# Optimization experiments

Hardware: AMD Instinct MI355X
Metric: run time of the kernel (lower is better)

## Reference

```python
import jax, jax.numpy as jnp
import numpy as np

# Model dims (match init_kwargs)
D_MODEL = 2048
H = 16        # query heads
HKV = 4       # kv heads (GQA)
DS = 32       # semantic head dim (compressed)
DG = 32       # geometric head dim (compressed, RoPE'd)
DV = 64       # value head dim
B, T = 2, 4096
MB = 64       # mem_block
LW = 1024     # local_window
ROPE_BASE = 10000.0
NEG_INF = -1e9


def _rope(x, pos, base):
    # x: [B, h, T, d] with d even; standard rotate-half RoPE
    d = x.shape[-1]
    inv_freq = 1.0 / (base ** (jnp.arange(0, d, 2, dtype=jnp.float32) / d))
    ang = pos.astype(jnp.float32)[:, None] * inv_freq          # [T, d/2]
    cos, sin = jnp.cos(ang), jnp.sin(ang)                      # [T, d/2]
    x1, x2 = jnp.split(x, 2, axis=-1)
    return jnp.concatenate([x1 * cos - x2 * sin,
                            x2 * cos + x1 * sin], axis=-1)


def setup_inputs() -> dict:
    key = jax.random.key(0)
    ks = jax.random.split(key, 8)
    w = lambda k, sh: jax.random.normal(k, sh, jnp.float32) * 0.02
    return {
        "x": jax.random.normal(ks[0], (B, T, D_MODEL), jnp.float32),
        "Wq_sem": w(ks[1], (D_MODEL, H * DS)),
        "Wk_sem": w(ks[2], (D_MODEL, HKV * DS)),
        "Wq_geo": w(ks[3], (D_MODEL, H * DG)),
        "Wk_geo": w(ks[4], (D_MODEL, HKV * DG)),
        "Wv": w(ks[5], (D_MODEL, HKV * DV)),
        "Wo": w(ks[6], (H * DV, D_MODEL)),
        "logit_scale": jnp.zeros((H,), jnp.float32),
    }


def reference(x, Wq_sem, Wk_sem, Wq_geo, Wk_geo, Wv, Wo, logit_scale):
    Bq, Tq = x.shape[0], x.shape[1]
    split = lambda y, h, d: y.reshape(Bq, Tq, h, d).transpose(0, 2, 1, 3)
    # Decoupled projections
    q_sem = split(x @ Wq_sem, H, DS)      # [B,H,T,DS]
    k_sem = split(x @ Wk_sem, HKV, DS)    # [B,HKV,T,DS]
    q_geo = split(x @ Wq_geo, H, DG)
    k_geo = split(x @ Wk_geo, HKV, DG)
    v = split(x @ Wv, HKV, DV)            # [B,HKV,T,DV]
    pos = jnp.arange(Tq)
    # RoPE only on the geometric path
    q_geo = _rope(q_geo, pos, ROPE_BASE)
    k_geo = _rope(k_geo, pos, ROPE_BASE)
    # Memory-block summarization: mean-pool remote KV into one token per block
    remote = Tq - LW
    nblk = remote // MB
    pool = lambda a: jnp.concatenate(
        [a[:, :, :remote].reshape(Bq, HKV, nblk, MB, a.shape[-1]).mean(axis=3),
         a[:, :, remote:]], axis=2)
    k_sem2, k_geo2, v2 = pool(k_sem), pool(k_geo), pool(v)  # [B,HKV,K,*], K=nblk+LW
    k_pos = jnp.concatenate([jnp.arange(nblk) * MB + (MB - 1),
                             jnp.arange(remote, Tq)])        # [K]
    # GQA head-group broadcast
    rep = lambda a: jnp.repeat(a, H // HKV, axis=1)
    k_sem2, k_geo2, v2 = rep(k_sem2), rep(k_geo2), rep(v2)   # [B,H,K,*]
    # Decoupled scores: semantic + geometric, each with its own scale
    scores = (jnp.einsum('bhqd,bhkd->bhqk', q_sem, k_sem2) * (1.0 / jnp.sqrt(float(DS)))
              + jnp.einsum('bhqd,bhkd->bhqk', q_geo, k_geo2) * (1.0 / jnp.sqrt(float(DG))))
    # Learned per-head temperature
    scores = scores * jnp.exp(logit_scale)[None, :, None, None]
    # Causal mask over summarized key positions
    mask = k_pos[None, :] <= pos[:, None]                    # [T,K]
    scores = jnp.where(mask[None, None], scores, NEG_INF)
    probs = jax.nn.softmax(scores, axis=-1)
    out = jnp.einsum('bhqk,bhkd->bhqd', probs, v2)           # [B,H,T,DV]
    out = out.transpose(0, 2, 1, 3).reshape(Bq, Tq, H * DV)
    return out @ Wo                                          # [B,T,D_MODEL]
```

## Files before the change

kernel.cpp:

```cpp
#include <hip/hip_runtime.h>
#include <math.h>

#define B_  2
#define T_  4096
#define DM  2048
#define H_  16
#define HKV 4
#define DV_ 64
#define MB_ 64
#define LW_ 1024
#define REMOTE 3072
#define NBLK 48
#define KTOT 1072
#define NTILES 17

typedef __bf16 bf16x8 __attribute__((ext_vector_type(8)));
typedef float  f32x4  __attribute__((ext_vector_type(4)));

__device__ __forceinline__ float bf2f(unsigned short u) {
    unsigned int x = ((unsigned int)u) << 16;
    return __builtin_bit_cast(float, x);
}
__device__ __forceinline__ unsigned short f2bf(float f) {
    unsigned int x = __builtin_bit_cast(unsigned int, f);
    x = x + 0x7fffu + ((x >> 16) & 1u);
    return (unsigned short)(x >> 16);
}

__device__ __forceinline__ void gload16(const unsigned short* gsrc,
                                        unsigned short* ldst) {
    __builtin_amdgcn_global_load_lds(
        (const __attribute__((address_space(1))) void*)gsrc,
        (__attribute__((address_space(3))) void*)ldst,
        16, 0, 0);
}

__global__ void cvt_f32_to_bf16(const float* __restrict__ src,
                                unsigned short* __restrict__ dst, int n) {
    int i = (blockIdx.x * blockDim.x + threadIdx.x) * 4;
    if (i >= n) return;
    float4 v = *(const float4*)(src + i);
    ushort4 o;
    o.x = f2bf(v.x); o.y = f2bf(v.y); o.z = f2bf(v.z); o.w = f2bf(v.w);
    *(ushort4*)(dst + i) = o;
}

__global__ void transpose_cvt(const float* __restrict__ src,
                              unsigned short* __restrict__ dst, int R, int C) {
    __shared__ float tile[32][33];
    int ct = blockIdx.x, rt = blockIdx.y;
    int tx = threadIdx.x, ty = threadIdx.y;
    #pragma unroll
    for (int i = ty; i < 32; i += 8)
        tile[i][tx] = src[(size_t)(rt * 32 + i) * C + ct * 32 + tx];
    __syncthreads();
    #pragma unroll
    for (int i = ty; i < 32; i += 8)
        dst[(size_t)(ct * 32 + i) * R + rt * 32 + tx] = f2bf(tile[tx][i]);
}

template<int MODE>
__global__ __launch_bounds__(256, 3) void gemmP(
    const unsigned short* __restrict__ A,
    const unsigned short* __restrict__ BT,
    float* __restrict__ outF,
    unsigned short* __restrict__ qcat,
    unsigned short* __restrict__ kcatf,
    unsigned short* __restrict__ vf,
    int M, int N, int K, int nbx)
{
    extern __shared__ __align__(16) unsigned short lds[];

    const int tid = threadIdx.x;
    const int lane = tid & 63, w = tid >> 6;
    const int wr = w >> 1, wc = w & 1;
    const int l15 = lane & 15, lg = lane >> 4;

    const int cpx = gridDim.x >> 3;
    const int swz = (blockIdx.x & 7) * cpx + (blockIdx.x >> 3);
    const int bx = swz % nbx, by = swz / nbx;
    const int row0 = by * 128, col0 = bx * 128;

    const int scol = ((lane & 3) ^ ((lane >> 3) & 3)) * 8;
    const int srA = w * 16 + (lane >> 2);
    const unsigned short* Ag = A  + (size_t)row0 * K;
    const unsigned short* Bg = BT + (size_t)col0 * K;

    const int rdsw = (lg ^ ((l15 >> 1) & 3)) * 8;
    const int aoff = (wr * 64 + l15) * 32 + rdsw;
    const int boff = (wc * 64 + l15) * 32 + rdsw;

    const int NT = K >> 5;
    f32x4 acc[4][4] = {};

    auto stage = [&](int s, int kk) {
        unsigned short* sa = lds + s * 8192;
        unsigned short* sb = sa + 4096;
        #pragma unroll
        for (int j = 0; j < 2; j++) {
            gload16(Ag + (size_t)(srA + j * 64) * K + kk + scol,
                    sa + (j * 256 + w * 64) * 8);
            gload16(Bg + (size_t)(srA + j * 64) * K + kk + scol,
                    sb + (j * 256 + w * 64) * 8);
        }
    };

    stage(0, 0);
    stage(1, 32);
    asm volatile("s_waitcnt vmcnt(4)" ::: "memory");

    int rs = 0;
    for (int t = 0; t < NT; ++t) {
        __builtin_amdgcn_s_barrier();
        const bool st = (t + 2) < NT;
        if (st) stage(rs == 0 ? 2 : rs - 1, (t + 2) << 5);

        const unsigned short* As_ = lds + rs * 8192;
        const unsigned short* Bs_ = As_ + 4096;
        bf16x8 af[4], bfr[4];
        #pragma unroll
        for (int mf = 0; mf < 4; mf++)
            af[mf] = __builtin_bit_cast(bf16x8, *(const uint4*)&As_[aoff + mf * 512]);
        #pragma unroll
        for (int nf = 0; nf < 4; nf++)
            bfr[nf] = __builtin_bit_cast(bf16x8, *(const uint4*)&Bs_[boff + nf * 512]);

        __builtin_amdgcn_s_setprio(1);
        #pragma unroll
        for (int mf = 0; mf < 4; mf++)
            #pragma unroll
            for (int nf = 0; nf < 4; nf++)
                acc[mf][nf] = __builtin_amdgcn_mfma_f32_16x16x32_bf16(
                                  af[mf], bfr[nf], acc[mf][nf], 0, 0, 0);
        __builtin_amdgcn_s_setprio(0);

        if (st) asm volatile("s_waitcnt vmcnt(4)" ::: "memory");
        else    asm volatile("s_waitcnt vmcnt(0)" ::: "memory");
        rs = (rs == 2) ? 0 : rs + 1;
    }

    #pragma unroll
    for (int mf = 0; mf < 4; mf++) {
        #pragma unroll
        for (int nf = 0; nf < 4; nf++) {
            #pragma unroll
            for (int r = 0; r < 4; r++) {
                int row = row0 + wr * 64 + mf * 16 + lg * 4 + r;
                int col = col0 + wc * 64 + nf * 16 + l15;
                float v = acc[mf][nf][r];
                if (MODE == 1) {
                    outF[(size_t)row * N + col] = v;
                } else {
                    int b = row >> 12, t = row & 4095;
                    unsigned short hv = f2bf(v);
                    if (col < 512) {
                        int h = col >> 5, d = col & 31;
                        qcat[(((size_t)(b*16 + h))*4096 + t)*64 + d] = hv;
                    } else if (col < 1024) {
                        int c2 = col - 512; int h = c2 >> 5, d = c2 & 31;
                        qcat[(((size_t)(b*16 + h))*4096 + t)*64 + 32 + d] = hv;
                    } else if (col < 1152) {
                        int c2 = col - 1024; int g = c2 >> 5, d = c2 & 31;
                        kcatf[(((size_t)(b*4 + g))*4096 + t)*64 + d] = hv;
                    } else if (col < 1280) {
                        int c2 = col - 1152; int g = c2 >> 5, d = c2 & 31;
                        kcatf[(((size_t)(b*4 + g))*4096 + t)*64 + 32 + d] = hv;
                    } else {
                        int c2 = col - 1280; int g = c2 >> 6, d = c2 & 63;
                        vf[(((size_t)(b*4 + g))*4096 + t)*64 + d] = hv;
                    }
                }
            }
        }
    }
}

__global__ void rope_rotate(unsigned short* __restrict__ buf, int nrows, int T) {
    int idx = blockIdx.x * 256 + threadIdx.x;
    int row = idx >> 4, i = idx & 15;
    if (row >= nrows) return;
    int t = row % T;
    float inv = exp2f(-(float)i * 0.8304820237218406f);
    float ang = (float)t * inv;
    float s, c;
    sincosf(ang, &s, &c);
    unsigned short* p = buf + (size_t)row * 64;
    float g1 = bf2f(p[32 + i]), g2 = bf2f(p[48 + i]);
    p[32 + i] = f2bf(g1 * c - g2 * s);
    p[48 + i] = f2bf(g2 * c + g1 * s);
}

__global__ void pool_kv(const unsigned short* __restrict__ kf,
                        const unsigned short* __restrict__ vfull,
                        unsigned short* __restrict__ kp,
                        unsigned short* __restrict__ vt) {
    int key = blockIdx.x % KTOT;
    int bg  = blockIdx.x / KTOT;
    int d = threadIdx.x;
    size_t srcbase = (size_t)bg * T_ * 64;
    size_t kdst = ((size_t)bg * KTOT + key) * 64 + d;
    size_t vdst = ((size_t)bg * 64 + d) * KTOT + key;
    if (key < NBLK) {
        float sk = 0.f, sv = 0.f;
        for (int j = 0; j < MB_; j++) {
            size_t o = srcbase + (size_t)(key * MB_ + j) * 64 + d;
            sk += bf2f(kf[o]);
            sv += bf2f(vfull[o]);
        }
        kp[kdst] = f2bf(sk * (1.f / 64.f));
        vt[vdst] = f2bf(sv * (1.f / 64.f));
    } else {
        int t = REMOTE + key - NBLK;
        size_t o = srcbase + (size_t)t * 64 + d;
        kp[kdst] = kf[o];
        vt[vdst] = vfull[o];
    }
}

__global__ __launch_bounds__(256) void attn_fwd(
    const unsigned short* __restrict__ qcat,
    const unsigned short* __restrict__ kp,
    const unsigned short* __restrict__ vt,
    const float* __restrict__ ls,
    unsigned short* __restrict__ attn_out)
{
    __shared__ unsigned short Pl[4][32][72];

    const int tid = threadIdx.x;
    const int lane = tid & 63, w = tid >> 6;
    const int l15 = lane & 15, lg = lane >> 4;

    const int wid = blockIdx.x * 4 + w;
    const int hb = wid & 31;
    const int iu = wid >> 5;
    int i;
    if (iu < 32)       i = 127 - iu;
    else if (iu == 32) i = 0;
    else if (iu == 33) i = 1;
    else               i = iu - 32;
    const int h = hb & 15, b = hb >> 4, g = h >> 2;
    const int q0 = i * 32;

    int ktmax;
    if (q0 < 64) ktmax = NTILES;
    else {
        int lastkey = q0 + 31 - 3024;
        ktmax = (lastkey < NBLK) ? 1 : (lastkey / 64 + 1);
    }

    const float sc = __expf(ls[h]) * 0.17677669529663687f;

    bf16x8 aq[2][2];
    const unsigned short* qbase = qcat + (((size_t)(b * 16 + h)) * T_ + q0) * 64;
    #pragma unroll
    for (int rf = 0; rf < 2; rf++)
        #pragma unroll
        for (int kh = 0; kh < 2; kh++)
            aq[rf][kh] = __builtin_bit_cast(bf16x8,
                *(const uint4*)(qbase + (size_t)(rf*16 + l15)*64 + kh*32 + lg*8));

    float m[2][4], lrun[2][4];
    #pragma unroll
    for (int rf = 0; rf < 2; rf++)
        #pragma unroll
        for (int r = 0; r < 4; r++) { m[rf][r] = -1e9f; lrun[rf][r] = 0.f; }
    f32x4 oacc[2][4] = {};

    const unsigned short* kbase = kp + ((size_t)(b * 4 + g)) * KTOT * 64;
    const unsigned short* vbase = vt + ((size_t)(b * 4 + g)) * 64 * KTOT;

    for (int kt = 0; kt < ktmax; kt++) {
        const int kb = kt * 64;

        bf16x8 bk[4][2];
        #pragma unroll
        for (int nf = 0; nf < 4; nf++) {
            int krow = kb + nf*16 + l15;
            int krc = krow < KTOT ? krow : KTOT - 1;
            #pragma unroll
            for (int kh = 0; kh < 2; kh++)
                bk[nf][kh] = __builtin_bit_cast(bf16x8,
                    *(const uint4*)(kbase + (size_t)krc * 64 + kh*32 + lg*8));
        }

        f32x4 s[2][4] = {};
        #pragma unroll
        for (int rf = 0; rf < 2; rf++)
            #pragma unroll
            for (int nf = 0; nf < 4; nf++)
                #pragma unroll
                for (int kh = 0; kh < 2; kh++)
                    s[rf][nf] = __builtin_amdgcn_mfma_f32_16x16x32_bf16(
                                    aq[rf][kh], bk[nf][kh], s[rf][nf], 0, 0, 0);

        bf16x8 bv[4][2];
        #pragma unroll
        for (int nfv = 0; nfv < 4; nfv++)
            #pragma unroll
            for (int kh = 0; kh < 2; kh++) {
                int kc = kb + kh*32 + lg*8;
                int kcc = (kc + 8 <= KTOT) ? kc : KTOT - 8;
                bv[nfv][kh] = __builtin_bit_cast(bf16x8,
                    *(const uint4*)(vbase + (size_t)(nfv*16 + l15) * KTOT + kcc));
            }

        #pragma unroll
        for (int rf = 0; rf < 2; rf++) {
            #pragma unroll
            for (int r = 0; r < 4; r++) {
                const int qpos = q0 + rf*16 + lg*4 + r;
                float vals[4];
                float tmax = -INFINITY;
                #pragma unroll
                for (int nf = 0; nf < 4; nf++) {
                    int key = kb + nf*16 + l15;
                    float v = s[rf][nf][r] * sc;
                    int kpos = (key < NBLK) ? key * 64 + 63 : 3024 + key;
                    v = (key < KTOT) ? ((kpos <= qpos) ? v : -1e9f) : -INFINITY;
                    vals[nf] = v;
                    tmax = fmaxf(tmax, v);
                }
                #pragma unroll
                for (int d = 1; d < 16; d <<= 1)
                    tmax = fmaxf(tmax, __shfl_xor(tmax, d));
                float mn = fmaxf(m[rf][r], tmax);
                float scl = __expf(m[rf][r] - mn);
                m[rf][r] = mn;
                float rs = 0.f;
                #pragma unroll
                for (int nf = 0; nf < 4; nf++) {
                    unsigned short pb = f2bf(__expf(vals[nf] - mn));
                    rs += bf2f(pb);
                    Pl[w][rf*16 + lg*4 + r][nf*16 + l15] = pb;
                }
                #pragma unroll
                for (int d = 1; d < 16; d <<= 1)
                    rs += __shfl_xor(rs, d);
                lrun[rf][r] = lrun[rf][r] * scl + rs;
                #pragma unroll
                for (int nfv = 0; nfv < 4; nfv++)
                    oacc[rf][nfv][r] *= scl;
            }
        }

        #pragma unroll
        for (int rf = 0; rf < 2; rf++) {
            bf16x8 pa[2];
            #pragma unroll
            for (int kh = 0; kh < 2; kh++)
                pa[kh] = __builtin_bit_cast(bf16x8,
                    *(const uint4*)&Pl[w][rf*16 + l15][kh*32 + lg*8]);
            #pragma unroll
            for (int nfv = 0; nfv < 4; nfv++)
                #pragma unroll
                for (int kh = 0; kh < 2; kh++)
                    oacc[rf][nfv] = __builtin_amdgcn_mfma_f32_16x16x32_bf16(
                                        pa[kh], bv[nfv][kh], oacc[rf][nfv], 0, 0, 0);
        }
    }

    #pragma unroll
    for (int rf = 0; rf < 2; rf++) {
        #pragma unroll
        for (int r = 0; r < 4; r++) {
            float inv = 1.f / lrun[rf][r];
            int q = q0 + rf*16 + lg*4 + r;
            size_t obase = ((size_t)(b * T_ + q)) * 1024 + h * 64;
            #pragma unroll
            for (int nfv = 0; nfv < 4; nfv++)
                attn_out[obase + nfv*16 + l15] = f2bf(oacc[rf][nfv][r] * inv);
        }
    }
}

extern "C" void kernel_launch(void* const* d_in, const int* in_sizes, int n_in,
                              void* d_out, int out_size, void* d_ws, size_t ws_size,
                              hipStream_t stream) {
    const float* x      = (const float*)d_in[0];
    const float* Wq_sem = (const float*)d_in[1];
    const float* Wk_sem = (const float*)d_in[2];
    const float* Wq_geo = (const float*)d_in[3];
    const float* Wk_geo = (const float*)d_in[4];
    const float* Wv     = (const float*)d_in[5];
    const float* Wo     = (const float*)d_in[6];
    const float* ls     = (const float*)d_in[7];

    char* w = (char*)d_ws;
    auto alloc = [&](size_t bytes) {
        char* p = w;
        w += (bytes + 255) & ~(size_t)255;
        return p;
    };
    unsigned short* xb    = (unsigned short*)alloc((size_t)8192 * 2048 * 2);
    unsigned short* WcatT = (unsigned short*)alloc((size_t)1536 * 2048 * 2);
    unsigned short* WoT   = (unsigned short*)alloc((size_t)2048 * 1024 * 2);
    unsigned short* qcat  = (unsigned short*)alloc((size_t)2 * 16 * 4096 * 64 * 2);
    unsigned short* kcatf = (unsigned short*)alloc((size_t)2 * 4 * 4096 * 64 * 2);
    unsigned short* vfull = (unsigned short*)alloc((size_t)2 * 4 * 4096 * 64 * 2);
    unsigned short* kcatp = (unsigned short*)alloc((size_t)2 * 4 * 1072 * 64 * 2);
    unsigned short* vpool = (unsigned short*)alloc((size_t)2 * 4 * 1072 * 64 * 2);
    unsigned short* aout  = (unsigned short*)alloc((size_t)8192 * 1024 * 2);

    hipFuncSetAttribute(reinterpret_cast<const void*>(&gemmP<0>),
                        hipFuncAttributeMaxDynamicSharedMemorySize, 49152);
    hipFuncSetAttribute(reinterpret_cast<const void*>(&gemmP<1>),
                        hipFuncAttributeMaxDynamicSharedMemorySize, 49152);

    cvt_f32_to_bf16<<<16384, 256, 0, stream>>>(x, xb, 8192 * 2048);

    dim3 tb(32, 8);
    transpose_cvt<<<dim3(16, 64), tb, 0, stream>>>(Wq_sem, WcatT + (size_t)0    * 2048, 2048, 512);
    transpose_cvt<<<dim3(16, 64), tb, 0, stream>>>(Wq_geo, WcatT + (size_t)512  * 2048, 2048, 512);
    transpose_cvt<<<dim3( 4, 64), tb, 0, stream>>>(Wk_sem, WcatT + (size_t)1024 * 2048, 2048, 128);
    transpose_cvt<<<dim3( 4, 64), tb, 0, stream>>>(Wk_geo, WcatT + (size_t)1152 * 2048, 2048, 128);
    transpose_cvt<<<dim3( 8, 64), tb, 0, stream>>>(Wv,     WcatT + (size_t)1280 * 2048, 2048, 256);
    transpose_cvt<<<dim3(64, 32), tb, 0, stream>>>(Wo, WoT, 1024, 2048);

    gemmP<0><<<768, 256, 49152, stream>>>(
        xb, WcatT, nullptr, qcat, kcatf, vfull, 8192, 1536, 2048, 12);

    rope_rotate<<<8192, 256, 0, stream>>>(qcat, 2 * 16 * 4096, 4096);
    rope_rotate<<<2048, 256, 0, stream>>>(kcatf, 2 * 4 * 4096, 4096);

    pool_kv<<<8 * KTOT, 64, 0, stream>>>(kcatf, vfull, kcatp, vpool);

    attn_fwd<<<dim3(1024), 256, 0, stream>>>(qcat, kcatp, vpool, ls, aout);

    gemmP<1><<<1024, 256, 49152, stream>>>(
        aout, WoT, (float*)d_out, nullptr, nullptr, nullptr, 8192, 2048, 1024, 16);
}
```

Baseline: 221.5 us.

## Fuse RoPE and KV mean-pooling into the projection GEMM epilogue

Result: faster. 203.4 us (-8.2%).

```diff
diff --git a/kernel.cpp b/kernel.cpp
--- a/kernel.cpp
+++ b/kernel.cpp
@@ -65,8 +65,8 @@
     const unsigned short* __restrict__ BT,
     float* __restrict__ outF,
     unsigned short* __restrict__ qcat,
-    unsigned short* __restrict__ kcatf,
-    unsigned short* __restrict__ vf,
+    unsigned short* __restrict__ kp,
+    unsigned short* __restrict__ vt,
     int M, int N, int K, int nbx)
 {
     extern __shared__ __align__(16) unsigned short lds[];
@@ -139,81 +139,102 @@
         rs = (rs == 2) ? 0 : rs + 1;
     }
 
-    #pragma unroll
-    for (int mf = 0; mf < 4; mf++) {
-        #pragma unroll
-        for (int nf = 0; nf < 4; nf++) {
-            #pragma unroll
-            for (int r = 0; r < 4; r++) {
-                int row = row0 + wr * 64 + mf * 16 + lg * 4 + r;
-                int col = col0 + wc * 64 + nf * 16 + l15;
-                float v = acc[mf][nf][r];
-                if (MODE == 1) {
-                    outF[(size_t)row * N + col] = v;
-                } else {
-                    int b = row >> 12, t = row & 4095;
-                    unsigned short hv = f2bf(v);
-                    if (col < 512) {
-                        int h = col >> 5, d = col & 31;
-                        qcat[(((size_t)(b*16 + h))*4096 + t)*64 + d] = hv;
-                    } else if (col < 1024) {
-                        int c2 = col - 512; int h = c2 >> 5, d = c2 & 31;
-                        qcat[(((size_t)(b*16 + h))*4096 + t)*64 + 32 + d] = hv;
-                    } else if (col < 1152) {
-                        int c2 = col - 1024; int g = c2 >> 5, d = c2 & 31;
-                        kcatf[(((size_t)(b*4 + g))*4096 + t)*64 + d] = hv;
-                    } else if (col < 1280) {
-                        int c2 = col - 1152; int g = c2 >> 5, d = c2 & 31;
-                        kcatf[(((size_t)(b*4 + g))*4096 + t)*64 + 32 + d] = hv;
+    if (MODE == 1) {
+        #pragma unroll
+        for (int mf = 0; mf < 4; mf++)
+            #pragma unroll
+            for (int nf = 0; nf < 4; nf++)
+                #pragma unroll
+                for (int r = 0; r < 4; r++) {
+                    int row = row0 + wr * 64 + mf * 16 + lg * 4 + r;
+                    int col = col0 + wc * 64 + nf * 16 + l15;
+                    outF[(size_t)row * N + col] = acc[mf][nf][r];
+                }
+    } else {
+        const int cspan = col0 + wc * 64;
+        const int tbase = row0 & 4095;
+        const int bq = row0 >> 12;
+
+        if ((cspan >= 512 && cspan < 1024) || (cspan >= 1152 && cspan < 1280)) {
+            const float invf = exp2f(-(float)l15 * 0.8304820237218406f);
+            #pragma unroll
+            for (int mf = 0; mf < 4; mf++) {
+                #pragma unroll
+                for (int r = 0; r < 4; r++) {
+                    float s, c;
+                    sincosf((float)(tbase + wr*64 + mf*16 + lg*4 + r) * invf, &s, &c);
+                    float a0 = acc[mf][0][r], a1 = acc[mf][1][r];
+                    acc[mf][0][r] = a0 * c - a1 * s;
+                    acc[mf][1][r] = a1 * c + a0 * s;
+                    float a2 = acc[mf][2][r], a3 = acc[mf][3][r];
+                    acc[mf][2][r] = a2 * c - a3 * s;
+                    acc[mf][3][r] = a3 * c + a2 * s;
+                }
+            }
+        }
+
+        if (cspan < 1024) {
+            #pragma unroll
+            for (int nf = 0; nf < 4; nf++) {
+                int col = cspan + nf * 16 + l15;
+                int h = (col < 512) ? (col >> 5) : ((col - 512) >> 5);
+                int d = (col < 512) ? (col & 31) : (32 + (col & 31));
+                unsigned short* qb =
+                    qcat + (((size_t)(bq * 16 + h)) * 4096 + tbase) * 64 + d;
+                #pragma unroll
+                for (int mf = 0; mf < 4; mf++)
+                    #pragma unroll
+                    for (int r = 0; r < 4; r++)
+                        qb[(size_t)(wr*64 + mf*16 + lg*4 + r) * 64] =
+                            f2bf(acc[mf][nf][r]);
+            }
+        } else if (tbase >= REMOTE) {
+            #pragma unroll
+            for (int nf = 0; nf < 4; nf++) {
+                int col = cspan + nf * 16 + l15;
+                #pragma unroll
+                for (int mf = 0; mf < 4; mf++)
+                    #pragma unroll
+                    for (int r = 0; r < 4; r++) {
+                        int key = tbase + wr*64 + mf*16 + lg*4 + r - 3024;
+                        unsigned short hv = f2bf(acc[mf][nf][r]);
+                        if (col < 1280) {
+                            int g, dk;
+                            if (col < 1152) { g = (col - 1024) >> 5; dk = col & 31; }
+                            else            { g = (col - 1152) >> 5; dk = 32 + (col & 31); }
+                            kp[(((size_t)(bq*4 + g)) * KTOT + key) * 64 + dk] = hv;
+                        } else {
+                            int g = (col - 1280) >> 6, dv = col & 63;
+                            vt[(((size_t)(bq*4 + g)) * 64 + dv) * KTOT + key] = hv;
+                        }
+                    }
+            }
+        } else {
+            #pragma unroll
+            for (int nf = 0; nf < 4; nf++) {
+                float ps = 0.f;
+                #pragma unroll
+                for (int mf = 0; mf < 4; mf++)
+                    #pragma unroll
+                    for (int r = 0; r < 4; r++) ps += acc[mf][nf][r];
+                ps += __shfl_xor(ps, 16);
+                ps += __shfl_xor(ps, 32);
+                if (lane < 16) {
+                    int col = cspan + nf * 16 + l15;
+                    int key = (tbase >> 6) + wr;
+                    unsigned short hv = f2bf(ps * (1.f / 64.f));
+                    if (col < 1280) {
+                        int g, dk;
+                        if (col < 1152) { g = (col - 1024) >> 5; dk = col & 31; }
+                        else            { g = (col - 1152) >> 5; dk = 32 + (col & 31); }
+                        kp[(((size_t)(bq*4 + g)) * KTOT + key) * 64 + dk] = hv;
                     } else {
-                        int c2 = col - 1280; int g = c2 >> 6, d = c2 & 63;
-                        vf[(((size_t)(b*4 + g))*4096 + t)*64 + d] = hv;
+                        int g = (col - 1280) >> 6, dv = col & 63;
+                        vt[(((size_t)(bq*4 + g)) * 64 + dv) * KTOT + key] = hv;
                     }
                 }
             }
         }
-    }
-}
-
-__global__ void rope_rotate(unsigned short* __restrict__ buf, int nrows, int T) {
-    int idx = blockIdx.x * 256 + threadIdx.x;
-    int row = idx >> 4, i = idx & 15;
-    if (row >= nrows) return;
-    int t = row % T;
-    float inv = exp2f(-(float)i * 0.8304820237218406f);
-    float ang = (float)t * inv;
-    float s, c;
-    sincosf(ang, &s, &c);
-    unsigned short* p = buf + (size_t)row * 64;
-    float g1 = bf2f(p[32 + i]), g2 = bf2f(p[48 + i]);
-    p[32 + i] = f2bf(g1 * c - g2 * s);
-    p[48 + i] = f2bf(g2 * c + g1 * s);
-}
-
-__global__ void pool_kv(const unsigned short* __restrict__ kf,
-                        const unsigned short* __restrict__ vfull,
-                        unsigned short* __restrict__ kp,
-                        unsigned short* __restrict__ vt) {
-    int key = blockIdx.x % KTOT;
-    int bg  = blockIdx.x / KTOT;
-    int d = threadIdx.x;
-    size_t srcbase = (size_t)bg * T_ * 64;
-    size_t kdst = ((size_t)bg * KTOT + key) * 64 + d;
-    size_t vdst = ((size_t)bg * 64 + d) * KTOT + key;
-    if (key < NBLK) {
-        float sk = 0.f, sv = 0.f;
-        for (int j = 0; j < MB_; j++) {
-            size_t o = srcbase + (size_t)(key * MB_ + j) * 64 + d;
-            sk += bf2f(kf[o]);
-            sv += bf2f(vfull[o]);
-        }
-        kp[kdst] = f2bf(sk * (1.f / 64.f));
-        vt[vdst] = f2bf(sv * (1.f / 64.f));
-    } else {
-        int t = REMOTE + key - NBLK;
-        size_t o = srcbase + (size_t)t * 64 + d;
-        kp[kdst] = kf[o];
-        vt[vdst] = vfull[o];
     }
 }
 
@@ -395,10 +416,8 @@
     unsigned short* WcatT = (unsigned short*)alloc((size_t)1536 * 2048 * 2);
     unsigned short* WoT   = (unsigned short*)alloc((size_t)2048 * 1024 * 2);
     unsigned short* qcat  = (unsigned short*)alloc((size_t)2 * 16 * 4096 * 64 * 2);
-    unsigned short* kcatf = (unsigned short*)alloc((size_t)2 * 4 * 4096 * 64 * 2);
-    unsigned short* vfull = (unsigned short*)alloc((size_t)2 * 4 * 4096 * 64 * 2);
-    unsigned short* kcatp = (unsigned short*)alloc((size_t)2 * 4 * 1072 * 64 * 2);
-    unsigned short* vpool = (unsigned short*)alloc((size_t)2 * 4 * 1072 * 64 * 2);
+    unsigned short* kp    = (unsigned short*)alloc((size_t)2 * 4 * 1072 * 64 * 2);
+    unsigned short* vt    = (unsigned short*)alloc((size_t)2 * 4 * 1072 * 64 * 2);
     unsigned short* aout  = (unsigned short*)alloc((size_t)8192 * 1024 * 2);
 
     hipFuncSetAttribute(reinterpret_cast<const void*>(&gemmP<0>),
@@ -417,14 +436,9 @@
     transpose_cvt<<<dim3(64, 32), tb, 0, stream>>>(Wo, WoT, 1024, 2048);
 
     gemmP<0><<<768, 256, 49152, stream>>>(
-        xb, WcatT, nullptr, qcat, kcatf, vfull, 8192, 1536, 2048, 12);
-
-    rope_rotate<<<8192, 256, 0, stream>>>(qcat, 2 * 16 * 4096, 4096);
-    rope_rotate<<<2048, 256, 0, stream>>>(kcatf, 2 * 4 * 4096, 4096);
-
-    pool_kv<<<8 * KTOT, 64, 0, stream>>>(kcatf, vfull, kcatp, vpool);
-
-    attn_fwd<<<dim3(1024), 256, 0, stream>>>(qcat, kcatp, vpool, ls, aout);
+        xb, WcatT, nullptr, qcat, kp, vt, 8192, 1536, 2048, 12);
+
+    attn_fwd<<<dim3(1024), 256, 0, stream>>>(qcat, kp, vt, ls, aout);
 
     gemmP<1><<<1024, 256, 49152, stream>>>(
         aout, WoT, (float*)d_out, nullptr, nullptr, nullptr, 8192, 2048, 1024, 16);
```
